# Kernel optimization log

Hardware: AMD Instinct MI355X
Metric: run time of the kernel (lower is better)

## Reference

```python
import jax, jax.numpy as jnp
import numpy as np

N = 100000      # nodes
E = 1000000     # edges
IN_DIM = 128
OUT_DIM = 64
K = 4
ALPHA = 0.5
LAMBD = 1.0


def setup_inputs() -> dict:
    key = jax.random.key(0)
    k1, k2, k3, k4 = jax.random.split(key, 4)
    features = jax.random.normal(k1, (N, IN_DIM), dtype=jnp.float32)
    # xavier_uniform for Linear weight [out, in]
    limit = float(np.sqrt(6.0 / (IN_DIM + OUT_DIM)))
    W = jax.random.uniform(k2, (OUT_DIM, IN_DIM), dtype=jnp.float32,
                           minval=-limit, maxval=limit)
    b = jnp.zeros((OUT_DIM,), dtype=jnp.float32)
    src = jax.random.randint(k3, (E,), 0, N, dtype=jnp.int32)
    dst = jax.random.randint(k4, (E,), 0, N, dtype=jnp.int32)
    return {"features": features, "W": W, "b": b, "src": src, "dst": dst}


def reference(features, W, b, src, dst):
    # in-degrees = number of edges entering each node (dst occurrences)
    degs = jax.ops.segment_sum(jnp.ones((E,), jnp.float32), dst, num_segments=N)
    norm_lambd_1 = (LAMBD * degs + 1.0) ** (-1.0)          # [N]
    norm05 = jnp.sqrt(degs + 1.0)[:, None]                 # [N,1]
    norm_05 = jax.lax.rsqrt(degs + 1.0)[:, None]           # [N,1]
    norm_lambd_1 = norm_lambd_1[:, None]                   # [N,1]

    h = features @ W.T + b                                 # [N, OUT]
    h_pre = h
    h_initial = h * norm_lambd_1

    def step(carry, _):
        h, h_pre = carry
        hh = h * norm_05                                   # D^{-1/2} scaling
        agg = jax.ops.segment_sum(hh[src], dst, num_segments=N)  # SpMM (copy_u, sum)
        h2 = agg * norm_lambd_1 * norm05
        hn = ALPHA * LAMBD * h2 + (1.0 - ALPHA) * h_pre + ALPHA * h_initial
        return (hn, hn), None

    (h, _), _ = jax.lax.scan(step, (h, h_pre), None, length=K)
    return h
```

## Files before the change

kernel.cpp:

```cpp
#include <hip/hip_runtime.h>

#define NN 100000
#define NE 1000000
#define IND 128
#define OUTD 64
#define KST 4
#define GM 64
#define MAXDEG 64
#define GEMM_BLKS ((NN + GM - 1) / GM)
#define BUCK_BLKS ((NE + 255) / 256)
#define FUSE_GRPS 782

typedef float vf4 __attribute__((ext_vector_type(4)));
typedef short bf8 __attribute__((ext_vector_type(8)));
typedef unsigned int u32;

__device__ __forceinline__ unsigned short f2bf(float f) {
    unsigned int x = __float_as_uint(f);
    return (unsigned short)((x + 0x7fffu + ((x >> 16) & 1u)) >> 16);
}
__device__ __forceinline__ unsigned int packbf(float a, float b) {
    return (unsigned int)f2bf(a) | ((unsigned int)f2bf(b) << 16);
}
__device__ __forceinline__ float lo16(unsigned int u) { return __uint_as_float(u << 16); }
__device__ __forceinline__ float hi16(unsigned int u) { return __uint_as_float(u & 0xffff0000u); }


__global__ void k_zero(int* __restrict__ cnt) {
    int i = blockIdx.x * 256 + threadIdx.x;
    if (i < NN) cnt[i] = 0;
}


__global__ __launch_bounds__(256) void k_build_gemm(
        const float* __restrict__ feat, const float* __restrict__ W,
        const float* __restrict__ bias,
        unsigned short* __restrict__ hraw16,
        const int* __restrict__ src, const int* __restrict__ dst,
        int* __restrict__ cnt, int* __restrict__ colidx) {
    int g = blockIdx.x / 7, m = blockIdx.x % 7;
    if (m >= 2) {
        int b = g * 5 + (m - 2);
        if (b < BUCK_BLKS) {
            int e = b * 256 + threadIdx.x;
            if (e < NE) {
                int d = dst[e];
                int rank = atomicAdd(&cnt[d], 1);
                if (rank < MAXDEG) colidx[d * MAXDEG + rank] = src[e];
            }
        }
        return;
    }
    int gb = g * 2 + m;
    if (gb >= GEMM_BLKS) return;

    __shared__ u32 Fl[GM * 64];
    __shared__ u32 Wl[OUTD * 64];
    int t = threadIdx.x;
    int n0 = gb * GM;

#pragma unroll
    for (int i = 0; i < 4; ++i) {
        int c = t + i * 256;
        int row = c >> 4, kc8 = c & 15;
        vf4 x0 = ((const vf4*)W)[row * 32 + kc8 * 2];
        vf4 x1 = ((const vf4*)W)[row * 32 + kc8 * 2 + 1];
        uint4 p;
        p.x = packbf(x0.x, x0.y); p.y = packbf(x0.z, x0.w);
        p.z = packbf(x1.x, x1.y); p.w = packbf(x1.z, x1.w);
        *(uint4*)((char*)Wl + row * 256 + ((kc8 ^ (row & 7)) << 4)) = p;
    }
#pragma unroll
    for (int i = 0; i < 4; ++i) {
        int c = t + i * 256;
        int row = c >> 4, kc8 = c & 15;
        int n = n0 + row;
        vf4 x0 = (vf4)(0.0f), x1 = (vf4)(0.0f);
        if (n < NN) {
            x0 = __builtin_nontemporal_load(&((const vf4*)feat)[n * 32 + kc8 * 2]);
            x1 = __builtin_nontemporal_load(&((const vf4*)feat)[n * 32 + kc8 * 2 + 1]);
        }
        uint4 p;
        p.x = packbf(x0.x, x0.y); p.y = packbf(x0.z, x0.w);
        p.z = packbf(x1.x, x1.y); p.w = packbf(x1.z, x1.w);
        *(uint4*)((char*)Fl + row * 256 + ((kc8 ^ (row & 7)) << 4)) = p;
    }
    __syncthreads();

    int lane = t & 63, wv = t >> 6;
    int mrow = lane & 15, q = lane >> 4;
    vf4 acc[4];
#pragma unroll
    for (int ct = 0; ct < 4; ++ct) acc[ct] = (vf4)(0.0f);

    int arow = wv * 16 + mrow;
#pragma unroll
    for (int kc = 0; kc < 4; ++kc) {
        bf8 a = *(const bf8*)((const char*)Fl + arow * 256 +
                              (((kc * 4 + q) ^ (arow & 7)) << 4));
#pragma unroll
        for (int ct = 0; ct < 4; ++ct) {
            int ch = ct * 16 + mrow;
            bf8 b = *(const bf8*)((const char*)Wl + ch * 256 +
                                  (((kc * 4 + q) ^ (ch & 7)) << 4));
            acc[ct] = __builtin_amdgcn_mfma_f32_16x16x32_bf16(a, b, acc[ct], 0, 0, 0);
        }
    }

    float bv[4];
#pragma unroll
    for (int ct = 0; ct < 4; ++ct) bv[ct] = bias[ct * 16 + mrow];

#pragma unroll
    for (int reg = 0; reg < 4; ++reg) {
        int n = n0 + wv * 16 + q * 4 + reg;
        if (n < NN) {
#pragma unroll
            for (int ct = 0; ct < 4; ++ct) {
                int ch = ct * 16 + mrow;
                hraw16[(size_t)n * OUTD + ch] = f2bf(acc[ct][reg] + bv[ct]);
            }
        }
    }
}


__global__ __launch_bounds__(256) void k_finish(const int* __restrict__ cnt,
                                                const unsigned short* __restrict__ hraw16,
                                                float* __restrict__ r,
                                                unsigned short* __restrict__ g16,
                                                unsigned short* __restrict__ hinit16) {
    int i = blockIdx.x * 256 + threadIdx.x;
    if (i >= NN * 16) return;
    int v = i >> 4, c4 = i & 15;
    float rv = rsqrtf((float)cnt[v] + 1.0f);
    if (c4 == 0) r[v] = rv;
    float s = rv * rv;
    size_t base = (size_t)v * OUTD + c4 * 4;
    uint2 hw = *(const uint2*)(hraw16 + base);
    float h0v = lo16(hw.x), h1 = hi16(hw.x), h2 = lo16(hw.y), h3 = hi16(hw.y);
    uint2 pg, pi;
    pg.x = packbf(h0v * rv, h1 * rv);
    pg.y = packbf(h2 * rv, h3 * rv);
    pi.x = packbf(h0v * s, h1 * s);
    pi.y = packbf(h2 * s, h3 * s);
    *(uint2*)(g16 + base)     = pg;
    *(uint2*)(hinit16 + base) = pi;
}


template<bool FINAL>
__global__ __launch_bounds__(256) void k_gather16(
        float* __restrict__ hn, unsigned short* __restrict__ gn16,
        const unsigned short* __restrict__ g16,
        const unsigned short* __restrict__ hinit16,
        const float* __restrict__ r, const int* __restrict__ cnt,
        const int* __restrict__ colidx) {
    int t = blockIdx.x * 256 + threadIdx.x;
    int wave = t >> 6;
    int lane = t & 63;
    int q  = lane >> 3;
    int c8 = lane & 7;
    int v = wave * 8 + q;
    bool valid = v < NN;
    int vc = valid ? v : NN - 1;
    int deg = min(cnt[vc], MAXDEG);
    if (!valid) deg = 0;
    int beg = vc * MAXDEG;
    int md = deg;
    md = max(md, __shfl_xor(md, 8, 64));
    md = max(md, __shfl_xor(md, 16, 64));
    md = max(md, __shfl_xor(md, 32, 64));

    float a0 = 0.f, a1 = 0.f, a2 = 0.f, a3 = 0.f;
    float a4 = 0.f, a5 = 0.f, a6 = 0.f, a7 = 0.f;
    int nb = (md + 7) >> 3;
    for (int b = 0; b < nb; ++b) {
        int kb = b * 8;
        uint4 u[8];
#pragma unroll
        for (int j = 0; j < 8; ++j) {
            int k = kb + j;
            int s = (k < deg) ? colidx[beg + k] : 0;
            u[j] = *(const uint4*)(g16 + (size_t)s * OUTD + 8 * c8);
        }
#pragma unroll
        for (int j = 0; j < 8; ++j) {
            if (kb + j < deg) {
                a0 += lo16(u[j].x); a1 += hi16(u[j].x);
                a2 += lo16(u[j].y); a3 += hi16(u[j].y);
                a4 += lo16(u[j].z); a5 += hi16(u[j].z);
                a6 += lo16(u[j].w); a7 += hi16(u[j].w);
            }
        }
    }

    if (valid) {
        float rv = r[v];
        float ir2 = 0.5f / rv;
        float hr  = 0.5f * rv;
        size_t base = (size_t)v * OUTD + 8 * c8;
        uint4 gs = *(const uint4*)(g16 + base);
        uint4 iv = *(const uint4*)(hinit16 + base);
        float o0 = fmaf(hr, a0, fmaf(lo16(gs.x), ir2, 0.5f * lo16(iv.x)));
        float o1 = fmaf(hr, a1, fmaf(hi16(gs.x), ir2, 0.5f * hi16(iv.x)));
        float o2 = fmaf(hr, a2, fmaf(lo16(gs.y), ir2, 0.5f * lo16(iv.y)));
        float o3 = fmaf(hr, a3, fmaf(hi16(gs.y), ir2, 0.5f * hi16(iv.y)));
        float o4 = fmaf(hr, a4, fmaf(lo16(gs.z), ir2, 0.5f * lo16(iv.z)));
        float o5 = fmaf(hr, a5, fmaf(hi16(gs.z), ir2, 0.5f * hi16(iv.z)));
        float o6 = fmaf(hr, a6, fmaf(lo16(gs.w), ir2, 0.5f * lo16(iv.w)));
        float o7 = fmaf(hr, a7, fmaf(hi16(gs.w), ir2, 0.5f * hi16(iv.w)));
        if (FINAL) {
            vf4 w0 = { o0, o1, o2, o3 };
            vf4 w1 = { o4, o5, o6, o7 };
            __builtin_nontemporal_store(w0, (vf4*)(hn + base));
            __builtin_nontemporal_store(w1, (vf4*)(hn + base + 4));
        } else {
            uint4 p;
            p.x = packbf(o0 * rv, o1 * rv);
            p.y = packbf(o2 * rv, o3 * rv);
            p.z = packbf(o4 * rv, o5 * rv);
            p.w = packbf(o6 * rv, o7 * rv);
            *(uint4*)(gn16 + base) = p;
        }
    }
}


extern "C" void kernel_launch(void* const* d_in, const int* in_sizes, int n_in,
                              void* d_out, int out_size, void* d_ws, size_t ws_size,
                              hipStream_t stream) {
    const float* feat = (const float*)d_in[0];
    const float* W    = (const float*)d_in[1];
    const float* bias = (const float*)d_in[2];
    const int*   src  = (const int*)d_in[3];
    const int*   dst  = (const int*)d_in[4];

    char* ws = (char*)d_ws;
    int*            cnt     = (int*)(ws + 0);
    float*          rr      = (float*)(ws + 400000);
    int*            colidx  = (int*)(ws + 800000);
    unsigned short* hraw16  = (unsigned short*)(ws + 26400000);
    unsigned short* g16A    = (unsigned short*)(ws + 39200000);
    unsigned short* g16B    = (unsigned short*)(ws + 52000000);
    unsigned short* hinit16 = (unsigned short*)(ws + 64800000);

    k_zero<<<(NN + 255) / 256, 256, 0, stream>>>(cnt);

    k_build_gemm<<<FUSE_GRPS * 7, 256, 0, stream>>>(
        feat, W, bias, hraw16, src, dst, cnt, colidx);

    k_finish<<<(NN * 16 + 255) / 256, 256, 0, stream>>>(
        cnt, hraw16, rr, g16A, hinit16);

    int gth_blocks = (NN + 31) / 32;
    k_gather16<false><<<gth_blocks, 256, 0, stream>>>(
        nullptr, g16B, g16A, hinit16, rr, cnt, colidx);
    k_gather16<false><<<gth_blocks, 256, 0, stream>>>(
        nullptr, g16A, g16B, hinit16, rr, cnt, colidx);
    k_gather16<false><<<gth_blocks, 256, 0, stream>>>(
        nullptr, g16B, g16A, hinit16, rr, cnt, colidx);
    k_gather16<true><<<gth_blocks, 256, 0, stream>>>(
        (float*)d_out, nullptr, g16B, hinit16, rr, cnt, colidx);
}
```

Measured before the change: 175.7 us.

## Drop finish kernel; compute degree scaling on the fly inside gather

Removes the k_finish pass and the separate pre-scaled and initial-state buffers. Each gather now stores the unscaled state and recomputes rsqrt(deg+1) per neighbor by gathering cnt[src], so the first gather can read the GEMM output directly. The zero kernel is also replaced with hipMemsetAsync. This saves one full-array pass and several buffers, but adds a scattered 4-byte cnt load and an rsqrt per edge in every iteration.

```diff
diff --git a/kernel.cpp b/kernel.cpp
--- a/kernel.cpp
+++ b/kernel.cpp
@@ -4,7 +4,6 @@
 #define NE 1000000
 #define IND 128
 #define OUTD 64
-#define KST 4
 #define GM 64
 #define MAXDEG 64
 #define GEMM_BLKS ((NN + GM - 1) / GM)
@@ -26,16 +25,10 @@
 __device__ __forceinline__ float hi16(unsigned int u) { return __uint_as_float(u & 0xffff0000u); }
 
 
-__global__ void k_zero(int* __restrict__ cnt) {
-    int i = blockIdx.x * 256 + threadIdx.x;
-    if (i < NN) cnt[i] = 0;
-}
-
-
 __global__ __launch_bounds__(256) void k_build_gemm(
         const float* __restrict__ feat, const float* __restrict__ W,
         const float* __restrict__ bias,
-        unsigned short* __restrict__ hraw16,
+        unsigned short* __restrict__ h016,
         const int* __restrict__ src, const int* __restrict__ dst,
         int* __restrict__ cnt, int* __restrict__ colidx) {
     int g = blockIdx.x / 7, m = blockIdx.x % 7;
@@ -118,44 +111,19 @@
 #pragma unroll
             for (int ct = 0; ct < 4; ++ct) {
                 int ch = ct * 16 + mrow;
-                hraw16[(size_t)n * OUTD + ch] = f2bf(acc[ct][reg] + bv[ct]);
+                h016[(size_t)n * OUTD + ch] = f2bf(acc[ct][reg] + bv[ct]);
             }
         }
     }
 }
 
 
-__global__ __launch_bounds__(256) void k_finish(const int* __restrict__ cnt,
-                                                const unsigned short* __restrict__ hraw16,
-                                                float* __restrict__ r,
-                                                unsigned short* __restrict__ g16,
-                                                unsigned short* __restrict__ hinit16) {
-    int i = blockIdx.x * 256 + threadIdx.x;
-    if (i >= NN * 16) return;
-    int v = i >> 4, c4 = i & 15;
-    float rv = rsqrtf((float)cnt[v] + 1.0f);
-    if (c4 == 0) r[v] = rv;
-    float s = rv * rv;
-    size_t base = (size_t)v * OUTD + c4 * 4;
-    uint2 hw = *(const uint2*)(hraw16 + base);
-    float h0v = lo16(hw.x), h1 = hi16(hw.x), h2 = lo16(hw.y), h3 = hi16(hw.y);
-    uint2 pg, pi;
-    pg.x = packbf(h0v * rv, h1 * rv);
-    pg.y = packbf(h2 * rv, h3 * rv);
-    pi.x = packbf(h0v * s, h1 * s);
-    pi.y = packbf(h2 * s, h3 * s);
-    *(uint2*)(g16 + base)     = pg;
-    *(uint2*)(hinit16 + base) = pi;
-}
-
-
-template<bool FINAL>
+template<bool FIRST, bool FINAL>
 __global__ __launch_bounds__(256) void k_gather16(
         float* __restrict__ hn, unsigned short* __restrict__ gn16,
-        const unsigned short* __restrict__ g16,
-        const unsigned short* __restrict__ hinit16,
-        const float* __restrict__ r, const int* __restrict__ cnt,
-        const int* __restrict__ colidx) {
+        const unsigned short* __restrict__ st16,
+        const unsigned short* __restrict__ h016,
+        const int* __restrict__ cnt, const int* __restrict__ colidx) {
     int t = blockIdx.x * 256 + threadIdx.x;
     int wave = t >> 6;
     int lane = t & 63;
@@ -164,7 +132,9 @@
     int v = wave * 8 + q;
     bool valid = v < NN;
     int vc = valid ? v : NN - 1;
-    int deg = min(cnt[vc], MAXDEG);
+    int dc = cnt[vc];
+    float rv = rsqrtf((float)dc + 1.0f);
+    int deg = min(dc, MAXDEG);
     if (!valid) deg = 0;
     int beg = vc * MAXDEG;
     int md = deg;
@@ -177,39 +147,43 @@
     int nb = (md + 7) >> 3;
     for (int b = 0; b < nb; ++b) {
         int kb = b * 8;
-        uint4 u[8];
+        int sj[8]; int cj[8]; uint4 u[8];
 #pragma unroll
         for (int j = 0; j < 8; ++j) {
             int k = kb + j;
-            int s = (k < deg) ? colidx[beg + k] : 0;
-            u[j] = *(const uint4*)(g16 + (size_t)s * OUTD + 8 * c8);
+            sj[j] = (k < deg) ? colidx[beg + k] : 0;
+        }
+#pragma unroll
+        for (int j = 0; j < 8; ++j) {
+            u[j]  = *(const uint4*)(st16 + (size_t)sj[j] * OUTD + 8 * c8);
+            cj[j] = cnt[sj[j]];
         }
 #pragma unroll
         for (int j = 0; j < 8; ++j) {
             if (kb + j < deg) {
-                a0 += lo16(u[j].x); a1 += hi16(u[j].x);
-                a2 += lo16(u[j].y); a3 += hi16(u[j].y);
-                a4 += lo16(u[j].z); a5 += hi16(u[j].z);
-                a6 += lo16(u[j].w); a7 += hi16(u[j].w);
+                float rs = rsqrtf((float)cj[j] + 1.0f);
+                a0 = fmaf(rs, lo16(u[j].x), a0); a1 = fmaf(rs, hi16(u[j].x), a1);
+                a2 = fmaf(rs, lo16(u[j].y), a2); a3 = fmaf(rs, hi16(u[j].y), a3);
+                a4 = fmaf(rs, lo16(u[j].z), a4); a5 = fmaf(rs, hi16(u[j].z), a5);
+                a6 = fmaf(rs, lo16(u[j].w), a6); a7 = fmaf(rs, hi16(u[j].w), a7);
             }
         }
     }
 
     if (valid) {
-        float rv = r[v];
-        float ir2 = 0.5f / rv;
         float hr  = 0.5f * rv;
+        float s2h = 0.5f * rv * rv;
         size_t base = (size_t)v * OUTD + 8 * c8;
-        uint4 gs = *(const uint4*)(g16 + base);
-        uint4 iv = *(const uint4*)(hinit16 + base);
-        float o0 = fmaf(hr, a0, fmaf(lo16(gs.x), ir2, 0.5f * lo16(iv.x)));
-        float o1 = fmaf(hr, a1, fmaf(hi16(gs.x), ir2, 0.5f * hi16(iv.x)));
-        float o2 = fmaf(hr, a2, fmaf(lo16(gs.y), ir2, 0.5f * lo16(iv.y)));
-        float o3 = fmaf(hr, a3, fmaf(hi16(gs.y), ir2, 0.5f * hi16(iv.y)));
-        float o4 = fmaf(hr, a4, fmaf(lo16(gs.z), ir2, 0.5f * lo16(iv.z)));
-        float o5 = fmaf(hr, a5, fmaf(hi16(gs.z), ir2, 0.5f * hi16(iv.z)));
-        float o6 = fmaf(hr, a6, fmaf(lo16(gs.w), ir2, 0.5f * lo16(iv.w)));
-        float o7 = fmaf(hr, a7, fmaf(hi16(gs.w), ir2, 0.5f * hi16(iv.w)));
+        uint4 us = *(const uint4*)(st16 + base);
+        uint4 u0 = FIRST ? us : *(const uint4*)(h016 + base);
+        float o0 = fmaf(hr, a0, fmaf(s2h, lo16(u0.x), 0.5f * lo16(us.x)));
+        float o1 = fmaf(hr, a1, fmaf(s2h, hi16(u0.x), 0.5f * hi16(us.x)));
+        float o2 = fmaf(hr, a2, fmaf(s2h, lo16(u0.y), 0.5f * lo16(us.y)));
+        float o3 = fmaf(hr, a3, fmaf(s2h, hi16(u0.y), 0.5f * hi16(us.y)));
+        float o4 = fmaf(hr, a4, fmaf(s2h, lo16(u0.z), 0.5f * lo16(us.z)));
+        float o5 = fmaf(hr, a5, fmaf(s2h, hi16(u0.z), 0.5f * hi16(us.z)));
+        float o6 = fmaf(hr, a6, fmaf(s2h, lo16(u0.w), 0.5f * lo16(us.w)));
+        float o7 = fmaf(hr, a7, fmaf(s2h, hi16(u0.w), 0.5f * hi16(us.w)));
         if (FINAL) {
             vf4 w0 = { o0, o1, o2, o3 };
             vf4 w1 = { o4, o5, o6, o7 };
@@ -217,10 +191,10 @@
             __builtin_nontemporal_store(w1, (vf4*)(hn + base + 4));
         } else {
             uint4 p;
-            p.x = packbf(o0 * rv, o1 * rv);
-            p.y = packbf(o2 * rv, o3 * rv);
-            p.z = packbf(o4 * rv, o5 * rv);
-            p.w = packbf(o6 * rv, o7 * rv);
+            p.x = packbf(o0, o1);
+            p.y = packbf(o2, o3);
+            p.z = packbf(o4, o5);
+            p.w = packbf(o6, o7);
             *(uint4*)(gn16 + base) = p;
         }
     }
@@ -237,29 +211,24 @@
     const int*   dst  = (const int*)d_in[4];
 
     char* ws = (char*)d_ws;
-    int*            cnt     = (int*)(ws + 0);
-    float*          rr      = (float*)(ws + 400000);
-    int*            colidx  = (int*)(ws + 800000);
-    unsigned short* hraw16  = (unsigned short*)(ws + 26400000);
-    unsigned short* g16A    = (unsigned short*)(ws + 39200000);
-    unsigned short* g16B    = (unsigned short*)(ws + 52000000);
-    unsigned short* hinit16 = (unsigned short*)(ws + 64800000);
-
-    k_zero<<<(NN + 255) / 256, 256, 0, stream>>>(cnt);
+    int*            cnt    = (int*)(ws + 0);
+    int*            colidx = (int*)(ws + 400000);
+    unsigned short* h016   = (unsigned short*)(ws + 26000000);
+    unsigned short* hA     = (unsigned short*)(ws + 38800000);
+    unsigned short* hB     = (unsigned short*)(ws + 51600000);
+
+    hipMemsetAsync(cnt, 0, NN * sizeof(int), stream);
 
     k_build_gemm<<<FUSE_GRPS * 7, 256, 0, stream>>>(
-        feat, W, bias, hraw16, src, dst, cnt, colidx);
-
-    k_finish<<<(NN * 16 + 255) / 256, 256, 0, stream>>>(
-        cnt, hraw16, rr, g16A, hinit16);
+        feat, W, bias, h016, src, dst, cnt, colidx);
 
     int gth_blocks = (NN + 31) / 32;
-    k_gather16<false><<<gth_blocks, 256, 0, stream>>>(
-        nullptr, g16B, g16A, hinit16, rr, cnt, colidx);
-    k_gather16<false><<<gth_blocks, 256, 0, stream>>>(
-        nullptr, g16A, g16B, hinit16, rr, cnt, colidx);
-    k_gather16<false><<<gth_blocks, 256, 0, stream>>>(
-        nullptr, g16B, g16A, hinit16, rr, cnt, colidx);
-    k_gather16<true><<<gth_blocks, 256, 0, stream>>>(
-        (float*)d_out, nullptr, g16B, hinit16, rr, cnt, colidx);
-}
+    k_gather16<true,  false><<<gth_blocks, 256, 0, stream>>>(
+        nullptr, hA, h016, h016, cnt, colidx);
+    k_gather16<false, false><<<gth_blocks, 256, 0, stream>>>(
+        nullptr, hB, hA, h016, cnt, colidx);
+    k_gather16<false, false><<<gth_blocks, 256, 0, stream>>>(
+        nullptr, hA, hB, h016, cnt, colidx);
+    k_gather16<false, true><<<gth_blocks, 256, 0, stream>>>(
+        (float*)d_out, nullptr, hA, h016, cnt, colidx);
+}
```

After: 178.8 us. About the same (+1.7%).
